# Performance work log

Hardware: AMD Instinct MI355X
Metric: run time of the kernel (lower is better)

The kernel has to match this reference:

```python
import jax, jax.numpy as jnp
import numpy as np

N_NODES = 100000
N_EDGES = 1600000
DIM = 128
HEADS = 8
PHC = DIM // HEADS  # per-head channels = 16


def setup_inputs() -> dict:
    key = jax.random.key(0)
    k1, k2, k3, k4, k5 = jax.random.split(key, 5)
    nodes = jax.random.normal(k1, (N_NODES, DIM), dtype=jnp.float32)
    senders = jax.random.randint(k2, (N_EDGES,), 0, N_NODES, dtype=jnp.int32)
    receivers = jax.random.randint(k3, (N_EDGES,), 0, N_NODES, dtype=jnp.int32)
    # VarianceScaling(fan_avg, uniform) ~ limit = sqrt(3/fan_avg)
    lim_w = np.sqrt(3.0 / DIM)
    W = jax.random.uniform(k4, (DIM, DIM), minval=-lim_w, maxval=lim_w, dtype=jnp.float32)
    b = jnp.zeros((DIM,), dtype=jnp.float32)
    lim_a = np.sqrt(3.0 * 2.0 / (2 * PHC + 1))
    attn_w = jax.random.uniform(k5, (2 * PHC, 1), minval=-lim_a, maxval=lim_a, dtype=jnp.float32)
    attn_b = jnp.zeros((1,), dtype=jnp.float32)
    return {"nodes": nodes, "senders": senders, "receivers": receivers,
            "W": W, "b": b, "attn_w": attn_w, "attn_b": attn_b}


def reference(nodes, senders, receivers, W, b, attn_w, attn_b):
    n = nodes.shape[0]
    # linear transform + split heads: [N, H, PHC]
    nt = (nodes @ W + b).reshape(n, HEADS, PHC)
    sent = nt[senders]      # [E, H, PHC] gather
    recv = nt[receivers]    # [E, H, PHC] gather
    # attention logits: Linear(1) over leaky_relu(concat(q,k)) -> [E, H, 1]
    qk = jax.nn.leaky_relu(jnp.concatenate([sent, recv], axis=-1), negative_slope=0.2)
    logits = qk @ attn_w + attn_b  # [E, H, 1]
    # segment softmax over edges grouped by receiver node
    seg_max = jax.ops.segment_max(logits, receivers, num_segments=n)  # [N, H, 1]
    exp = jnp.exp(logits - seg_max[receivers])
    denom = jax.ops.segment_sum(exp, receivers, num_segments=n)  # [N, H, 1]
    alpha = exp / denom[receivers]
    # weighted scatter-sum of sender features
    out = jax.ops.segment_sum(sent * alpha, receivers, num_segments=n)  # [N, H, PHC]
    return out.reshape(n, -1)  # concat=True -> [N, DIM]
```

## Files before the change

kernel.cpp:

```cpp
#include <hip/hip_runtime.h>

#define DIM 128
#define HEADS 8
#define PHC 16

#define BSHIFT 6
#define BNODES 64
#define CAP 1408
#define NBMAX 1600

typedef __bf16 bf16x4 __attribute__((ext_vector_type(4)));
typedef __bf16 bf16x8 __attribute__((ext_vector_type(8)));
typedef float  f32x4  __attribute__((ext_vector_type(4)));

__device__ inline unsigned short f2bf(float x) {
  unsigned int u = __float_as_uint(x);
  unsigned int r = (u + 0x7FFF + ((u >> 16) & 1)) >> 16;
  return (unsigned short)r;
}

__global__ __launch_bounds__(256) void k_prepw(
    const float* __restrict__ W, __bf16* __restrict__ Wh,
    __bf16* __restrict__ Wl, int* __restrict__ gCursor, int NB) {
  const int tuple = blockIdx.x * 256 + threadIdx.x;
  if (tuple < NB) gCursor[tuple] = 0;
  const int ln = tuple & 15;
  const int lg = (tuple >> 4) & 3;
  const int cg = (tuple >> 6) & 7;
  const int kt = tuple >> 9;
  const int col = (cg << 4) + ln;
  bf16x8 h, l;
#pragma unroll
  for (int e = 0; e < 8; ++e) {
    int k = (kt << 5) + ((e >> 2) << 4) + (lg << 2) + (e & 3);
    float wv = W[k * DIM + col];
    __bf16 hh = (__bf16)wv;
    h[e] = hh;
    l[e] = (__bf16)(wv - (float)hh);
  }
  *(bf16x8*)(Wh + tuple * 8) = h;
  *(bf16x8*)(Wl + tuple * 8) = l;
}

#define GROWS 64

__global__ __launch_bounds__(256, 3) void k_gemm_scatter(
    const float* __restrict__ A, const __bf16* __restrict__ Wh,
    const __bf16* __restrict__ Wl, const float* __restrict__ bias,
    const float* __restrict__ attn_w, unsigned int* __restrict__ nt_hp,
    float* __restrict__ s_exp_hp, const int* __restrict__ send,
    const int* __restrict__ recv, int* __restrict__ gCursor,
    unsigned int* __restrict__ pairs, int E, int NB, int nScat, int n) {
  __shared__ __align__(16) float smemF[GROWS * DIM];

  if (blockIdx.x < nScat) {
    int* cnt = (int*)smemF;
    int* cur = cnt + NBMAX;
    const int t = threadIdx.x;
    for (int i = t; i < NB; i += 256) cnt[i] = 0;
    __syncthreads();
    const int e0 = blockIdx.x * 8192;
    const int e1 = min(e0 + 8192, E);
    for (int i = e0 + t; i < e1; i += 256)
      atomicAdd(&cnt[recv[i] >> BSHIFT], 1);
    __syncthreads();
    for (int i = t; i < NB; i += 256) {
      int c = cnt[i];
      cur[i] = i * CAP + (c ? atomicAdd(&gCursor[i], c) : 0);
    }
    __syncthreads();
    for (int i = e0 + t; i < e1; i += 256) {
      int r = recv[i];
      int b = r >> BSHIFT;
      int p = atomicAdd(&cur[b], 1);
      if (p - b * CAP < CAP)
        pairs[p] = (unsigned int)send[i] | ((unsigned int)(r & (BNODES - 1)) << 17);
    }
    return;
  }

  __bf16* Ah = (__bf16*)smemF;
  __bf16* Al = Ah + GROWS * DIM;
  const int t    = threadIdx.x;
  const int row0 = (blockIdx.x - nScat) * GROWS;
  const int lane = t & 63;
  const int w    = t >> 6;
  const int lg   = lane >> 4;
  const int ln   = lane & 15;

  float4 av[8];
  {
    const float4* A4 = (const float4*)(A + (size_t)row0 * DIM);
    const int lim = min(GROWS, n - row0) * (DIM / 4);
#pragma unroll
    for (int j = 0; j < 8; ++j) {
      int i = t + j * 256;
      av[j] = (i < lim) ? A4[i] : make_float4(0.f, 0.f, 0.f, 0.f);
    }
  }

#pragma unroll
  for (int j = 0; j < 8; ++j) {
    int i = t + j * 256;
    int r = i >> 5, c4 = i & 31;
    int ktc = c4 >> 3, lgc = c4 & 3, ehi = (c4 >> 2) & 1;
    int unit = (r << 4) + (((ktc << 2) + lgc) ^ (r & 15));
    int ei = (unit << 3) + (ehi << 2);
    float x0 = av[j].x, x1 = av[j].y, x2 = av[j].z, x3 = av[j].w;
    __bf16 h0 = (__bf16)x0, h1 = (__bf16)x1, h2 = (__bf16)x2, h3 = (__bf16)x3;
    bf16x4 hv = {h0, h1, h2, h3};
    bf16x4 lv = {(__bf16)(x0 - (float)h0), (__bf16)(x1 - (float)h1),
                 (__bf16)(x2 - (float)h2), (__bf16)(x3 - (float)h3)};
    *(bf16x4*)(Ah + ei) = hv;
    *(bf16x4*)(Al + ei) = lv;
  }

  f32x4 acc[4][2];
  {
    const float b0 = bias[(w << 5) + ln];
    const float b1 = bias[(w << 5) + 16 + ln];
#pragma unroll
    for (int rt = 0; rt < 4; ++rt) {
      acc[rt][0] = (f32x4){b0, b0, b0, b0};
      acc[rt][1] = (f32x4){b1, b1, b1, b1};
    }
  }
  __syncthreads();

  const int cg0 = w << 1;
#pragma unroll
  for (int kt = 0; kt < 4; ++kt) {
    bf16x8 Bh0, Bl0, Bh1, Bl1;
    {
      int i0 = ((((kt << 3) + cg0) << 2) + lg) * 16 + ln;
      int i1 = ((((kt << 3) + cg0 + 1) << 2) + lg) * 16 + ln;
      Bh0 = *(const bf16x8*)(Wh + (i0 << 3));
      Bl0 = *(const bf16x8*)(Wl + (i0 << 3));
      Bh1 = *(const bf16x8*)(Wh + (i1 << 3));
      Bl1 = *(const bf16x8*)(Wl + (i1 << 3));
    }
    bf16x8 ah[4], al[4];
#pragma unroll
    for (int rt = 0; rt < 4; ++rt) {
      int m = (rt << 4) + ln;
      int u = (m << 4) + (((kt << 2) + lg) ^ (m & 15));
      ah[rt] = *(const bf16x8*)(Ah + (u << 3));
      al[rt] = *(const bf16x8*)(Al + (u << 3));
    }
#pragma unroll
    for (int rt = 0; rt < 4; ++rt) {
      acc[rt][0] = __builtin_amdgcn_mfma_f32_16x16x32_bf16(ah[rt], Bh0, acc[rt][0], 0, 0, 0);
      acc[rt][0] = __builtin_amdgcn_mfma_f32_16x16x32_bf16(ah[rt], Bl0, acc[rt][0], 0, 0, 0);
      acc[rt][0] = __builtin_amdgcn_mfma_f32_16x16x32_bf16(al[rt], Bh0, acc[rt][0], 0, 0, 0);
      acc[rt][1] = __builtin_amdgcn_mfma_f32_16x16x32_bf16(ah[rt], Bh1, acc[rt][1], 0, 0, 0);
      acc[rt][1] = __builtin_amdgcn_mfma_f32_16x16x32_bf16(ah[rt], Bl1, acc[rt][1], 0, 0, 0);
      acc[rt][1] = __builtin_amdgcn_mfma_f32_16x16x32_bf16(al[rt], Bh1, acc[rt][1], 0, 0, 0);
    }
  }

  __syncthreads();

#pragma unroll
  for (int rt = 0; rt < 4; ++rt)
#pragma unroll
    for (int ct = 0; ct < 2; ++ct) {
      int colx = ((w << 5) + (ct << 4) + ln) ^ ((lg & 1) << 4);
#pragma unroll
      for (int r = 0; r < 4; ++r) {
        int rowl = (rt << 4) + (lg << 2) + r;
        smemF[(rowl << 7) + colx] = acc[rt][ct][r];
      }
    }

  {
    const float aw = attn_w[ln];
#pragma unroll
    for (int rt = 0; rt < 4; ++rt)
#pragma unroll
      for (int ct = 0; ct < 2; ++ct) {
#pragma unroll
        for (int r = 0; r < 4; ++r) {
          float v = acc[rt][ct][r];
          float p = (v > 0.f ? v : 0.2f * v) * aw;
          p += __shfl_xor(p, 1);
          p += __shfl_xor(p, 2);
          p += __shfl_xor(p, 4);
          p += __shfl_xor(p, 8);
          if (ln == 0) {
            int row = row0 + (rt << 4) + (lg << 2) + r;
            if (row < n) s_exp_hp[((size_t)w * n + row) * 2 + ct] = __expf(p);
          }
        }
      }
  }
  __syncthreads();

  {
    const int nrow = min(GROWS, n - row0);
    const int r = t >> 2;
    const int q = t & 3;
    if (r < nrow) {
#pragma unroll
      for (int j = 0; j < 8; ++j) {
        int c4 = (j << 2) + q;
        int c4s = c4 ^ (((r >> 2) & 1) << 2);
        f32x4 v = *(const f32x4*)(smemF + (r << 7) + (c4s << 2));
        unsigned int lo = (unsigned int)f2bf(v[0]) | ((unsigned int)f2bf(v[1]) << 16);
        unsigned int hi = (unsigned int)f2bf(v[2]) | ((unsigned int)f2bf(v[3]) << 16);
        ((uint2*)nt_hp)[((size_t)(j >> 1) * n + row0 + r) * 8 + (j & 1) * 4 + q] =
            make_uint2(lo, hi);
      }
    }
  }
}

__global__ __launch_bounds__(256) void k_buildcsr(
    const unsigned int* __restrict__ pairs, const int* __restrict__ gCursor,
    int* __restrict__ csr_g, unsigned int* __restrict__ meta_g) {
  __shared__ unsigned int buf[CAP];
  __shared__ int hist[BNODES], curl[BNODES];
  __shared__ unsigned int slotmeta[BNODES];
  const int b = blockIdx.x;
  const int t = threadIdx.x;
  const int base = b * CAP;
  const int bsize = min(gCursor[b], CAP);

  for (int i = t; i < bsize; i += 256) buf[i] = pairs[base + i];
  if (t < BNODES) hist[t] = 0;
  __syncthreads();
  for (int i = t; i < bsize; i += 256)
    atomicAdd(&hist[(buf[i] >> 17) & (BNODES - 1)], 1);
  __syncthreads();
  if (t < 64) {
    int v = hist[t];
    int x = v;
#pragma unroll
    for (int off = 1; off < 64; off <<= 1) {
      int y = __shfl_up(x, off);
      if (t >= off) x += y;
    }
    int e = x - v;
    curl[t] = e;
    int rank = 0;
    for (int j = 0; j < 64; ++j) {
      int dj = hist[j];
      rank += (dj > v) || (dj == v && j < t);
    }
    slotmeta[rank] = ((unsigned int)e << 17) | ((unsigned int)v << 6) |
                     (unsigned int)t;
  }
  __syncthreads();
  if (t < 64) meta_g[(b << 6) + t] = slotmeta[t];
  for (int i = t; i < bsize; i += 256) {
    unsigned int v = buf[i];
    int p = atomicAdd(&curl[(v >> 17) & (BNODES - 1)], 1);
    csr_g[base + p] = (int)(v & 0x1FFFF);
  }
}

__global__ __launch_bounds__(256) void k_agg(
    const int* __restrict__ csr_g, const int* __restrict__ gCursor,
    const unsigned int* __restrict__ meta_g, const unsigned int* __restrict__ nt_hp,
    const float* __restrict__ s_exp_hp, float* __restrict__ out, int n) {
  __shared__ int csr_l[CAP];
  __shared__ unsigned int smeta[BNODES];
  const int b  = blockIdx.x >> 2;
  const int hp = blockIdx.x & 3;
  const int t = threadIdx.x;
  const int bsize = min(gCursor[b], CAP);

  for (int i = t; i < bsize; i += 256)
    csr_l[i] = __builtin_nontemporal_load(&csr_g[b * CAP + i]);
  if (t < BNODES) smeta[t] = meta_g[(b << 6) + t];
  __syncthreads();

  const int lane8 = t & 7;
  const int par   = lane8 >> 2;
  const uint2* nt2 = (const uint2*)nt_hp;
  const size_t pb8 = (size_t)hp * n * 8;
  const float* spp = s_exp_hp + (size_t)hp * n * 2;

#pragma unroll 1
  for (int pi = 0; pi < 2; ++pi) {
    const int nl = (t >> 3) + (pi << 5);
    const unsigned int m = smeta[nl];
    const int node = (b << BSHIFT) + (int)(m & 63);
    const int deg  = (int)((m >> 6) & 0x7FF);
    const int eoff = (int)(m >> 17);
    f32x4 a = {0.f, 0.f, 0.f, 0.f};
    float den = 0.f;
    for (int j = 0; j < deg; j += 4) {
      bool ok1 = (j + 1) < deg, ok2 = (j + 2) < deg, ok3 = (j + 3) < deg;
      int s0 = csr_l[eoff + j];
      int s1 = csr_l[ok1 ? (eoff + j + 1) : eoff];
      int s2 = csr_l[ok2 ? (eoff + j + 2) : eoff];
      int s3 = csr_l[ok3 ? (eoff + j + 3) : eoff];
      float w0 = spp[s0 * 2 + par];
      float w1 = ok1 ? spp[s1 * 2 + par] : 0.f;
      float w2 = ok2 ? spp[s2 * 2 + par] : 0.f;
      float w3 = ok3 ? spp[s3 * 2 + par] : 0.f;
      uint2 q0 = nt2[pb8 + s0 * 8 + lane8];
      uint2 q1 = nt2[pb8 + s1 * 8 + lane8];
      uint2 q2 = nt2[pb8 + s2 * 8 + lane8];
      uint2 q3 = nt2[pb8 + s3 * 8 + lane8];
      den += (w0 + w1) + (w2 + w3);
      a.x = fmaf(w0, __uint_as_float(q0.x << 16),
            fmaf(w1, __uint_as_float(q1.x << 16),
            fmaf(w2, __uint_as_float(q2.x << 16),
            fmaf(w3, __uint_as_float(q3.x << 16), a.x))));
      a.y = fmaf(w0, __uint_as_float(q0.x & 0xFFFF0000u),
            fmaf(w1, __uint_as_float(q1.x & 0xFFFF0000u),
            fmaf(w2, __uint_as_float(q2.x & 0xFFFF0000u),
            fmaf(w3, __uint_as_float(q3.x & 0xFFFF0000u), a.y))));
      a.z = fmaf(w0, __uint_as_float(q0.y << 16),
            fmaf(w1, __uint_as_float(q1.y << 16),
            fmaf(w2, __uint_as_float(q2.y << 16),
            fmaf(w3, __uint_as_float(q3.y << 16), a.z))));
      a.w = fmaf(w0, __uint_as_float(q0.y & 0xFFFF0000u),
            fmaf(w1, __uint_as_float(q1.y & 0xFFFF0000u),
            fmaf(w2, __uint_as_float(q2.y & 0xFFFF0000u),
            fmaf(w3, __uint_as_float(q3.y & 0xFFFF0000u), a.w))));
    }
    if (node < n) {
      const float inv = (deg > 0) ? 1.0f / den : 0.f;
      f32x4 o = {a.x * inv, a.y * inv, a.z * inv, a.w * inv};
      __builtin_nontemporal_store(
          o, (f32x4*)out + (size_t)node * 32 + (hp << 3) + lane8);
    }
  }
}

extern "C" void kernel_launch(void* const* d_in, const int* in_sizes, int n_in,
                              void* d_out, int out_size, void* d_ws, size_t ws_size,
                              hipStream_t stream) {
  const float* nodes   = (const float*)d_in[0];
  const int*   senders = (const int*)d_in[1];
  const int*   recvs   = (const int*)d_in[2];
  const float* W       = (const float*)d_in[3];
  const float* bias    = (const float*)d_in[4];
  const float* attn_w  = (const float*)d_in[5];

  const int n = in_sizes[0] / DIM;
  const int E = in_sizes[1];
  const int NB = (n + BNODES - 1) >> BSHIFT;

  char* w = (char*)d_ws;
  auto align256 = [](size_t x) { return (x + 255) & ~(size_t)255; };
  size_t off = 0;
  unsigned int* nt_hp = (unsigned int*)(w + off); off += align256((size_t)n * DIM * 2);
  float* s_exp_hp = (float*)(w + off); off += align256((size_t)n * HEADS * 4);
  unsigned int* pairs = (unsigned int*)(w + off); off += align256((size_t)NB * CAP * 4);
  int* csr_g     = (int*)(w + off);   off += align256((size_t)NB * CAP * 4);
  unsigned int* meta_g = (unsigned int*)(w + off); off += align256((size_t)NB * 64 * 4);
  int* gCursor   = (int*)(w + off);   off += align256((size_t)NB * 4);
  __bf16* Wh     = (__bf16*)(w + off); off += align256((size_t)2048 * 8 * 2);
  __bf16* Wl     = (__bf16*)(w + off); off += align256((size_t)2048 * 8 * 2);
  (void)ws_size;

  k_prepw<<<8, 256, 0, stream>>>(W, Wh, Wl, gCursor, NB);
  const int nScat = (E + 8191) / 8192;
  const int ngemm = (n + GROWS - 1) / GROWS;
  k_gemm_scatter<<<nScat + ngemm, 256, 0, stream>>>(
      nodes, Wh, Wl, bias, attn_w, nt_hp, s_exp_hp,
      senders, recvs, gCursor, pairs, E, NB, nScat, n);
  k_buildcsr<<<NB, 256, 0, stream>>>(pairs, gCursor, csr_g, meta_g);
  k_agg<<<NB * 4, 256, 0, stream>>>(csr_g, gCursor, meta_g, nt_hp, s_exp_hp,
                                    (float*)d_out, n);
}
```

Before: 261.9 us.

## Fuse CSR build into aggregation kernel and unroll edge loop by eight

```diff
diff --git a/kernel.cpp b/kernel.cpp
--- a/kernel.cpp
+++ b/kernel.cpp
@@ -214,18 +214,22 @@
   }
 }
 
-__global__ __launch_bounds__(256) void k_buildcsr(
+__global__ __launch_bounds__(256) void k_aggbuild(
     const unsigned int* __restrict__ pairs, const int* __restrict__ gCursor,
-    int* __restrict__ csr_g, unsigned int* __restrict__ meta_g) {
+    const unsigned int* __restrict__ nt_hp, const float* __restrict__ s_exp_hp,
+    float* __restrict__ out, int n) {
   __shared__ unsigned int buf[CAP];
+  __shared__ int csr_l[CAP];
   __shared__ int hist[BNODES], curl[BNODES];
   __shared__ unsigned int slotmeta[BNODES];
-  const int b = blockIdx.x;
+  const int b  = blockIdx.x >> 2;
+  const int hp = blockIdx.x & 3;
   const int t = threadIdx.x;
   const int base = b * CAP;
   const int bsize = min(gCursor[b], CAP);
 
-  for (int i = t; i < bsize; i += 256) buf[i] = pairs[base + i];
+  for (int i = t; i < bsize; i += 256)
+    buf[i] = __builtin_nontemporal_load(&pairs[base + i]);
   if (t < BNODES) hist[t] = 0;
   __syncthreads();
   for (int i = t; i < bsize; i += 256)
@@ -250,28 +254,11 @@
                      (unsigned int)t;
   }
   __syncthreads();
-  if (t < 64) meta_g[(b << 6) + t] = slotmeta[t];
   for (int i = t; i < bsize; i += 256) {
     unsigned int v = buf[i];
     int p = atomicAdd(&curl[(v >> 17) & (BNODES - 1)], 1);
-    csr_g[base + p] = (int)(v & 0x1FFFF);
-  }
-}
-
-__global__ __launch_bounds__(256) void k_agg(
-    const int* __restrict__ csr_g, const int* __restrict__ gCursor,
-    const unsigned int* __restrict__ meta_g, const unsigned int* __restrict__ nt_hp,
-    const float* __restrict__ s_exp_hp, float* __restrict__ out, int n) {
-  __shared__ int csr_l[CAP];
-  __shared__ unsigned int smeta[BNODES];
-  const int b  = blockIdx.x >> 2;
-  const int hp = blockIdx.x & 3;
-  const int t = threadIdx.x;
-  const int bsize = min(gCursor[b], CAP);
-
-  for (int i = t; i < bsize; i += 256)
-    csr_l[i] = __builtin_nontemporal_load(&csr_g[b * CAP + i]);
-  if (t < BNODES) smeta[t] = meta_g[(b << 6) + t];
+    csr_l[p] = (int)(v & 0x1FFFF);
+  }
   __syncthreads();
 
   const int lane8 = t & 7;
@@ -283,43 +270,31 @@
 #pragma unroll 1
   for (int pi = 0; pi < 2; ++pi) {
     const int nl = (t >> 3) + (pi << 5);
-    const unsigned int m = smeta[nl];
+    const unsigned int m = slotmeta[nl];
     const int node = (b << BSHIFT) + (int)(m & 63);
     const int deg  = (int)((m >> 6) & 0x7FF);
     const int eoff = (int)(m >> 17);
     f32x4 a = {0.f, 0.f, 0.f, 0.f};
     float den = 0.f;
-    for (int j = 0; j < deg; j += 4) {
-      bool ok1 = (j + 1) < deg, ok2 = (j + 2) < deg, ok3 = (j + 3) < deg;
-      int s0 = csr_l[eoff + j];
-      int s1 = csr_l[ok1 ? (eoff + j + 1) : eoff];
-      int s2 = csr_l[ok2 ? (eoff + j + 2) : eoff];
-      int s3 = csr_l[ok3 ? (eoff + j + 3) : eoff];
-      float w0 = spp[s0 * 2 + par];
-      float w1 = ok1 ? spp[s1 * 2 + par] : 0.f;
-      float w2 = ok2 ? spp[s2 * 2 + par] : 0.f;
-      float w3 = ok3 ? spp[s3 * 2 + par] : 0.f;
-      uint2 q0 = nt2[pb8 + s0 * 8 + lane8];
-      uint2 q1 = nt2[pb8 + s1 * 8 + lane8];
-      uint2 q2 = nt2[pb8 + s2 * 8 + lane8];
-      uint2 q3 = nt2[pb8 + s3 * 8 + lane8];
-      den += (w0 + w1) + (w2 + w3);
-      a.x = fmaf(w0, __uint_as_float(q0.x << 16),
-            fmaf(w1, __uint_as_float(q1.x << 16),
-            fmaf(w2, __uint_as_float(q2.x << 16),
-            fmaf(w3, __uint_as_float(q3.x << 16), a.x))));
-      a.y = fmaf(w0, __uint_as_float(q0.x & 0xFFFF0000u),
-            fmaf(w1, __uint_as_float(q1.x & 0xFFFF0000u),
-            fmaf(w2, __uint_as_float(q2.x & 0xFFFF0000u),
-            fmaf(w3, __uint_as_float(q3.x & 0xFFFF0000u), a.y))));
-      a.z = fmaf(w0, __uint_as_float(q0.y << 16),
-            fmaf(w1, __uint_as_float(q1.y << 16),
-            fmaf(w2, __uint_as_float(q2.y << 16),
-            fmaf(w3, __uint_as_float(q3.y << 16), a.z))));
-      a.w = fmaf(w0, __uint_as_float(q0.y & 0xFFFF0000u),
-            fmaf(w1, __uint_as_float(q1.y & 0xFFFF0000u),
-            fmaf(w2, __uint_as_float(q2.y & 0xFFFF0000u),
-            fmaf(w3, __uint_as_float(q3.y & 0xFFFF0000u), a.w))));
+    for (int j = 0; j < deg; j += 8) {
+      int   ss[8];
+      float ww[8];
+      uint2 qq[8];
+#pragma unroll
+      for (int u = 0; u < 8; ++u) {
+        bool ok = (j + u) < deg;
+        ss[u] = csr_l[ok ? (eoff + j + u) : eoff];
+        ww[u] = ok ? spp[ss[u] * 2 + par] : 0.f;
+        qq[u] = nt2[pb8 + ss[u] * 8 + lane8];
+      }
+#pragma unroll
+      for (int u = 0; u < 8; ++u) {
+        den += ww[u];
+        a.x = fmaf(ww[u], __uint_as_float(qq[u].x << 16), a.x);
+        a.y = fmaf(ww[u], __uint_as_float(qq[u].x & 0xFFFF0000u), a.y);
+        a.z = fmaf(ww[u], __uint_as_float(qq[u].y << 16), a.z);
+        a.w = fmaf(ww[u], __uint_as_float(qq[u].y & 0xFFFF0000u), a.w);
+      }
     }
     if (node < n) {
       const float inv = (deg > 0) ? 1.0f / den : 0.f;
@@ -350,8 +325,6 @@
   unsigned int* nt_hp = (unsigned int*)(w + off); off += align256((size_t)n * DIM * 2);
   float* s_exp_hp = (float*)(w + off); off += align256((size_t)n * HEADS * 4);
   unsigned int* pairs = (unsigned int*)(w + off); off += align256((size_t)NB * CAP * 4);
-  int* csr_g     = (int*)(w + off);   off += align256((size_t)NB * CAP * 4);
-  unsigned int* meta_g = (unsigned int*)(w + off); off += align256((size_t)NB * 64 * 4);
   int* gCursor   = (int*)(w + off);   off += align256((size_t)NB * 4);
   __bf16* Wh     = (__bf16*)(w + off); off += align256((size_t)2048 * 8 * 2);
   __bf16* Wl     = (__bf16*)(w + off); off += align256((size_t)2048 * 8 * 2);
@@ -363,7 +336,6 @@
   k_gemm_scatter<<<nScat + ngemm, 256, 0, stream>>>(
       nodes, Wh, Wl, bias, attn_w, nt_hp, s_exp_hp,
       senders, recvs, gCursor, pairs, E, NB, nScat, n);
-  k_buildcsr<<<NB, 256, 0, stream>>>(pairs, gCursor, csr_g, meta_g);
-  k_agg<<<NB * 4, 256, 0, stream>>>(csr_g, gCursor, meta_g, nt_hp, s_exp_hp,
-                                    (float*)d_out, n);
-}
+  k_aggbuild<<<NB * 4, 256, 0, stream>>>(pairs, gCursor, nt_hp, s_exp_hp,
+                                         (float*)d_out, n);
+}
```

Measured after the change: 252.1 us. 1.04x faster.
